# Kernel optimization log

Measured on AMD Instinct MI355X. Metric: run time of the kernel, lower is better.

Reference implementation:

```python
import jax, jax.numpy as jnp
import numpy as np

MAGNITUDE = 9
PROB = 0.5
WARP_STRENGTH = MAGNITUDE * 0.3 / 9.0  # = 0.3


def _notaknot_matrix(S):
    # System for second derivatives M of a cubic spline on uniform grid h=1
    # (scipy CubicSpline default bc_type='not-a-knot').
    A = np.zeros((S, S), dtype=np.float32)
    i = np.arange(1, S - 1)
    A[i, i - 1] = 1.0
    A[i, i] = 4.0
    A[i, i + 1] = 1.0
    # not-a-knot: third derivative continuous at x1 and x_{S-2}
    A[0, 0], A[0, 1], A[0, 2] = 1.0, -2.0, 1.0
    A[-1, -3], A[-1, -2], A[-1, -1] = 1.0, -2.0, 1.0
    return A


def setup_inputs() -> dict:
    key = jax.random.key(0)
    k1, k2, k3 = jax.random.split(key, 3)
    B, C, S = 128, 64, 4096
    x = jax.random.normal(k1, (B, C, S), dtype=jnp.float32)
    # per-sample scale ~ U(1 - warp_strength, 1 + warp_strength)
    scale = (1.0 - WARP_STRENGTH) + 2.0 * WARP_STRENGTH * jax.random.uniform(k2, (B,), dtype=jnp.float32)
    # per-sample apply decision: rand < prob
    apply_mask = jax.random.uniform(k3, (B,)) < PROB
    return {"x": x, "scale": scale, "apply_mask": apply_mask}


def reference(x, scale, apply_mask):
    B, C, S = x.shape
    A = jnp.asarray(_notaknot_matrix(S))  # (S, S), fixed uniform-grid system

    # --- fit not-a-knot cubic splines for all B*C signals at once ---
    y = x.reshape(B * C, S)
    rhs = jnp.zeros_like(y).at[:, 1:-1].set(
        6.0 * (y[:, :-2] - 2.0 * y[:, 1:-1] + y[:, 2:])
    )  # not-a-knot rows have rhs 0
    M = jnp.linalg.solve(A, rhs.T).T.reshape(B, C, S)  # second derivatives

    # --- warped evaluation points (shared across channels of a sample) ---
    grid = jnp.arange(S, dtype=x.dtype)
    w = jnp.clip(grid[None, :] * scale[:, None], 0.0, S - 1)  # (B, S)
    idx = jnp.clip(jnp.floor(w).astype(jnp.int32), 0, S - 2)  # interval index
    t = (w - idx.astype(x.dtype))[:, None, :]                 # (B, 1, S)

    idx3 = jnp.broadcast_to(idx[:, None, :], (B, C, S))
    y0 = jnp.take_along_axis(x, idx3, axis=2)
    y1 = jnp.take_along_axis(x, idx3 + 1, axis=2)
    M0 = jnp.take_along_axis(M, idx3, axis=2)
    M1 = jnp.take_along_axis(M, idx3 + 1, axis=2)

    # s(t) = y0 + b t + c t^2 + d t^3 on each unit interval (h = 1)
    b = (y1 - y0) - (2.0 * M0 + M1) / 6.0
    c = M0 / 2.0
    d = (M1 - M0) / 6.0
    warped = y0 + t * (b + t * (c + t * d))

    return jnp.where(apply_mask[:, None, None], warped, x)
```

## Files before the change

### kernel.cpp

```cpp
#include <hip/hip_runtime.h>
#include <math.h>


#define SLEN 4096
#define WRAD 8
#define BLK  256

typedef float f32x4 __attribute__((ext_vector_type(4)));

__global__ __launch_bounds__(BLK, 5) void time_warp_kernel(
    const float* __restrict__ x,
    const float* __restrict__ scale,
    const int*   __restrict__ apply_mask,
    float* __restrict__ out,
    int C)
{
    __shared__ float sy[SLEN];
    __shared__ float sm[SLEN];

    const int bid = blockIdx.x;
    const int b   = bid / C;
    const int t   = threadIdx.x;
    const float* __restrict__ xin = x   + (size_t)bid * SLEN;
    float*       __restrict__ o   = out + (size_t)bid * SLEN;

    if (apply_mask[b] == 0) {
        const f32x4* __restrict__ xi4 = (const f32x4*)xin;
        f32x4*       __restrict__ o4  = (f32x4*)o;
        #pragma unroll
        for (int k = 0; k < 4; ++k) {
            f32x4 v = xi4[t + BLK * k];
            __builtin_nontemporal_store(v, &o4[t + BLK * k]);
        }
        return;
    }

    {
        const float4* __restrict__ xi4 = (const float4*)xin;
        #pragma unroll
        for (int k = 0; k < 4; ++k)
            *(float4*)&sy[4 * (t + BLK * k)] = xi4[t + BLK * k];
    }
    __syncthreads();

    const float r = 0.26794919243112270f;
    float G[WRAD + 1];
    G[0] = 0.28867513459481287f;
    #pragma unroll
    for (int k = 1; k <= WRAD; ++k) G[k] = -G[k - 1] * r;
    float Hh[WRAD + 2];
    Hh[0] = 12.0f * (G[1] - G[0]);
    #pragma unroll
    for (int k = 1; k < WRAD; ++k) Hh[k] = 6.0f * (G[k - 1] - 2.0f * G[k] + G[k + 1]);
    Hh[WRAD]     = 6.0f * (G[WRAD - 1] - 2.0f * G[WRAD]);
    Hh[WRAD + 1] = 6.0f * G[WRAD];
    const float log2r = -1.8999686269529532f;

    #pragma unroll
    for (int s = 0; s < 4; ++s) {
        const int j0 = 4 * t + 1024 * s;
        if (j0 >= 36 && j0 <= SLEN - 44) {
            float wv[28];
            #pragma unroll
            for (int m = 0; m < 7; ++m)
                *(float4*)&wv[4 * m] = *(const float4*)&sy[j0 - 12 + 4 * m];
            float mv[4];
            #pragma unroll
            for (int e = 0; e < 4; ++e) {
                float acc = Hh[0] * wv[12 + e];
                #pragma unroll
                for (int k = 1; k <= WRAD + 1; ++k)
                    acc += Hh[k] * (wv[12 + e - k] + wv[12 + e + k]);
                mv[e] = acc;
            }
            *(float4*)&sm[j0] = make_float4(mv[0], mv[1], mv[2], mv[3]);
        } else {
            const float M1  = sy[0]        - 2.0f * sy[1]        + sy[2];
            const float MS2 = sy[SLEN - 3] - 2.0f * sy[SLEN - 2] + sy[SLEN - 1];

            float v1 = 0.0f, vS2 = 0.0f;
            #pragma unroll
            for (int k = 1; k <= WRAD; ++k) {
                const int ja = 1 + k;
                float fa = 6.0f * (sy[ja - 1] - 2.0f * sy[ja] + sy[ja + 1]);
                if (ja == 2) fa -= M1;
                v1 += G[k] * fa;
                const int jb = SLEN - 2 - k;
                float fb = 6.0f * (sy[jb - 1] - 2.0f * sy[jb] + sy[jb + 1]);
                if (jb == SLEN - 3) fb -= MS2;
                vS2 += G[k] * fb;
            }

            float wv[28];
            #pragma unroll
            for (int m = 0; m < 7; ++m) {
                const int q = j0 - 12 + 4 * m;
                float4 v = make_float4(0.0f, 0.0f, 0.0f, 0.0f);
                if (q >= 0 && q <= SLEN - 4) v = *(const float4*)&sy[q];
                *(float4*)&wv[4 * m] = v;
            }
            float fw[20];
            #pragma unroll
            for (int p = 0; p < 20; ++p) {
                const int jj = j0 + p - 8;
                float fv = 6.0f * (wv[p + 3] - 2.0f * wv[p + 4] + wv[p + 5]);
                if (jj < 2 || jj > SLEN - 3) fv = 0.0f;
                if (jj == 2)        fv -= M1;
                if (jj == SLEN - 3) fv -= MS2;
                fw[p] = fv;
            }
            float mv[4];
            #pragma unroll
            for (int e = 0; e < 4; ++e) {
                float acc = G[0] * fw[8 + e];
                #pragma unroll
                for (int k = 1; k <= WRAD; ++k)
                    acc += G[k] * (fw[8 + e - k] + fw[8 + e + k]);
                const int i = j0 + e;
                if (i >= 2 && i <= 34) {
                    float cc = v1 * exp2f((float)(i - 1) * log2r);
                    acc += (i & 1) ? -cc : cc;
                }
                if (i >= SLEN - 36 && i <= SLEN - 3) {
                    float cc = vS2 * exp2f((float)(SLEN - 2 - i) * log2r);
                    acc += (i & 1) ? cc : -cc;
                }
                mv[e] = acc;
            }
            if (j0 == 0)        { mv[1] = M1;  mv[0] = 2.0f * M1  - mv[2]; }
            if (j0 == SLEN - 4) { mv[2] = MS2; mv[3] = 2.0f * MS2 - mv[1]; }
            *(float4*)&sm[j0] = make_float4(mv[0], mv[1], mv[2], mv[3]);
        }
    }
    __syncthreads();

    const float sc = scale[b];
    #pragma unroll
    for (int q = 0; q < 16; ++q) {
        const int j = t + BLK * q;
        float w = fminf((float)j * sc, (float)(SLEN - 1));
        int idx = (int)w;
        if (idx > SLEN - 2) idx = SLEN - 2;
        const float tt  = w - (float)idx;
        const float y0  = sy[idx];
        const float y1  = sy[idx + 1];
        const float m0  = sm[idx];
        const float m1v = sm[idx + 1];
        const float bb = (y1 - y0) - (2.0f * m0 + m1v) * (1.0f / 6.0f);
        const float cc = 0.5f * m0;
        const float dd = (m1v - m0) * (1.0f / 6.0f);
        const float res = y0 + tt * (bb + tt * (cc + tt * dd));
        __builtin_nontemporal_store(res, &o[j]);
    }
}

extern "C" void kernel_launch(void* const* d_in, const int* in_sizes, int n_in,
                              void* d_out, int out_size, void* d_ws, size_t ws_size,
                              hipStream_t stream) {
    const float* x     = (const float*)d_in[0];
    const float* scale = (const float*)d_in[1];
    const int*   mask  = (const int*)d_in[2];
    float*       out   = (float*)d_out;

    const int B     = in_sizes[1];
    const int total = in_sizes[0];
    const int C     = total / (B * SLEN);
    const int nblk  = B * C;

    time_warp_kernel<<<nblk, BLK, 0, stream>>>(x, scale, mask, out, C);
}
```

Measured before the change: 237.9 us.

## Use persistent blocks with register prefetch of the next signal

The per-signal grid becomes a persistent grid of 1280 blocks that loop over signals with a stride. Each block loads the next signal into registers while it computes the spline for the current one, so global load latency overlaps with compute. Custom barriers that only wait on LDS replace __syncthreads. Masked signals are now copied from shared memory rather than directly from global memory, and holding the prefetch registers may raise register pressure and limit occupancy.

```diff
diff --git a/kernel.cpp b/kernel.cpp
--- a/kernel.cpp
+++ b/kernel.cpp
@@ -5,43 +5,28 @@
 #define SLEN 4096
 #define WRAD 8
 #define BLK  256
+#define GRID 1280
 
 typedef float f32x4 __attribute__((ext_vector_type(4)));
+
+__device__ __forceinline__ void lbar() {
+    __builtin_amdgcn_sched_barrier(0);
+    asm volatile("s_waitcnt lgkmcnt(0)" ::: "memory");
+    __builtin_amdgcn_s_barrier();
+    __builtin_amdgcn_sched_barrier(0);
+}
 
 __global__ __launch_bounds__(BLK, 5) void time_warp_kernel(
     const float* __restrict__ x,
     const float* __restrict__ scale,
     const int*   __restrict__ apply_mask,
     float* __restrict__ out,
-    int C)
+    int C, int nsig)
 {
     __shared__ float sy[SLEN];
     __shared__ float sm[SLEN];
 
-    const int bid = blockIdx.x;
-    const int b   = bid / C;
-    const int t   = threadIdx.x;
-    const float* __restrict__ xin = x   + (size_t)bid * SLEN;
-    float*       __restrict__ o   = out + (size_t)bid * SLEN;
-
-    if (apply_mask[b] == 0) {
-        const f32x4* __restrict__ xi4 = (const f32x4*)xin;
-        f32x4*       __restrict__ o4  = (f32x4*)o;
-        #pragma unroll
-        for (int k = 0; k < 4; ++k) {
-            f32x4 v = xi4[t + BLK * k];
-            __builtin_nontemporal_store(v, &o4[t + BLK * k]);
-        }
-        return;
-    }
-
-    {
-        const float4* __restrict__ xi4 = (const float4*)xin;
-        #pragma unroll
-        for (int k = 0; k < 4; ++k)
-            *(float4*)&sy[4 * (t + BLK * k)] = xi4[t + BLK * k];
-    }
-    __syncthreads();
+    const int t = threadIdx.x;
 
     const float r = 0.26794919243112270f;
     float G[WRAD + 1];
@@ -56,101 +41,142 @@
     Hh[WRAD + 1] = 6.0f * G[WRAD];
     const float log2r = -1.8999686269529532f;
 
-    #pragma unroll
-    for (int s = 0; s < 4; ++s) {
-        const int j0 = 4 * t + 1024 * s;
-        if (j0 >= 36 && j0 <= SLEN - 44) {
-            float wv[28];
+    int bid = blockIdx.x;
+    f32x4 pf0, pf1, pf2, pf3;
+    if (bid < nsig) {
+        const f32x4* __restrict__ xi4 = (const f32x4*)(x + (size_t)bid * SLEN);
+        pf0 = xi4[t];
+        pf1 = xi4[t + BLK];
+        pf2 = xi4[t + 2 * BLK];
+        pf3 = xi4[t + 3 * BLK];
+    }
+
+    for (; bid < nsig; bid += GRID) {
+        const int   b   = bid / C;
+        const int   msk = apply_mask[b];
+        const float sc  = scale[b];
+        float* __restrict__ o = out + (size_t)bid * SLEN;
+
+        lbar();
+        *(f32x4*)&sy[4 * t]        = pf0;
+        *(f32x4*)&sy[4 * t + 1024] = pf1;
+        *(f32x4*)&sy[4 * t + 2048] = pf2;
+        *(f32x4*)&sy[4 * t + 3072] = pf3;
+        lbar();
+
+        const int nxt = bid + GRID;
+        if (nxt < nsig) {
+            const f32x4* __restrict__ xi4 = (const f32x4*)(x + (size_t)nxt * SLEN);
+            pf0 = xi4[t];
+            pf1 = xi4[t + BLK];
+            pf2 = xi4[t + 2 * BLK];
+            pf3 = xi4[t + 3 * BLK];
+        }
+
+        if (msk == 0) {
             #pragma unroll
-            for (int m = 0; m < 7; ++m)
-                *(float4*)&wv[4 * m] = *(const float4*)&sy[j0 - 12 + 4 * m];
-            float mv[4];
-            #pragma unroll
-            for (int e = 0; e < 4; ++e) {
-                float acc = Hh[0] * wv[12 + e];
+            for (int k = 0; k < 4; ++k) {
+                f32x4 v = *(const f32x4*)&sy[4 * (t + BLK * k)];
+                __builtin_nontemporal_store(v, &((f32x4*)o)[t + BLK * k]);
+            }
+            continue;
+        }
+
+        #pragma unroll
+        for (int s = 0; s < 4; ++s) {
+            const int j0 = 4 * t + 1024 * s;
+            if (j0 >= 36 && j0 <= SLEN - 44) {
+                float wv[28];
                 #pragma unroll
-                for (int k = 1; k <= WRAD + 1; ++k)
-                    acc += Hh[k] * (wv[12 + e - k] + wv[12 + e + k]);
-                mv[e] = acc;
+                for (int m = 0; m < 7; ++m)
+                    *(float4*)&wv[4 * m] = *(const float4*)&sy[j0 - 12 + 4 * m];
+                float mv[4];
+                #pragma unroll
+                for (int e = 0; e < 4; ++e) {
+                    float acc = Hh[0] * wv[12 + e];
+                    #pragma unroll
+                    for (int k = 1; k <= WRAD + 1; ++k)
+                        acc += Hh[k] * (wv[12 + e - k] + wv[12 + e + k]);
+                    mv[e] = acc;
+                }
+                *(float4*)&sm[j0] = make_float4(mv[0], mv[1], mv[2], mv[3]);
+            } else {
+                const float M1  = sy[0]        - 2.0f * sy[1]        + sy[2];
+                const float MS2 = sy[SLEN - 3] - 2.0f * sy[SLEN - 2] + sy[SLEN - 1];
+
+                float v1 = 0.0f, vS2 = 0.0f;
+                #pragma unroll
+                for (int k = 1; k <= WRAD; ++k) {
+                    const int ja = 1 + k;
+                    float fa = 6.0f * (sy[ja - 1] - 2.0f * sy[ja] + sy[ja + 1]);
+                    if (ja == 2) fa -= M1;
+                    v1 += G[k] * fa;
+                    const int jb = SLEN - 2 - k;
+                    float fb = 6.0f * (sy[jb - 1] - 2.0f * sy[jb] + sy[jb + 1]);
+                    if (jb == SLEN - 3) fb -= MS2;
+                    vS2 += G[k] * fb;
+                }
+
+                float wv[28];
+                #pragma unroll
+                for (int m = 0; m < 7; ++m) {
+                    const int q = j0 - 12 + 4 * m;
+                    float4 v = make_float4(0.0f, 0.0f, 0.0f, 0.0f);
+                    if (q >= 0 && q <= SLEN - 4) v = *(const float4*)&sy[q];
+                    *(float4*)&wv[4 * m] = v;
+                }
+                float fw[20];
+                #pragma unroll
+                for (int p = 0; p < 20; ++p) {
+                    const int jj = j0 + p - 8;
+                    float fv = 6.0f * (wv[p + 3] - 2.0f * wv[p + 4] + wv[p + 5]);
+                    if (jj < 2 || jj > SLEN - 3) fv = 0.0f;
+                    if (jj == 2)        fv -= M1;
+                    if (jj == SLEN - 3) fv -= MS2;
+                    fw[p] = fv;
+                }
+                float mv[4];
+                #pragma unroll
+                for (int e = 0; e < 4; ++e) {
+                    float acc = G[0] * fw[8 + e];
+                    #pragma unroll
+                    for (int k = 1; k <= WRAD; ++k)
+                        acc += G[k] * (fw[8 + e - k] + fw[8 + e + k]);
+                    const int i = j0 + e;
+                    if (i >= 2 && i <= 34) {
+                        float cc = v1 * exp2f((float)(i - 1) * log2r);
+                        acc += (i & 1) ? -cc : cc;
+                    }
+                    if (i >= SLEN - 36 && i <= SLEN - 3) {
+                        float cc = vS2 * exp2f((float)(SLEN - 2 - i) * log2r);
+                        acc += (i & 1) ? cc : -cc;
+                    }
+                    mv[e] = acc;
+                }
+                if (j0 == 0)        { mv[1] = M1;  mv[0] = 2.0f * M1  - mv[2]; }
+                if (j0 == SLEN - 4) { mv[2] = MS2; mv[3] = 2.0f * MS2 - mv[1]; }
+                *(float4*)&sm[j0] = make_float4(mv[0], mv[1], mv[2], mv[3]);
             }
-            *(float4*)&sm[j0] = make_float4(mv[0], mv[1], mv[2], mv[3]);
-        } else {
-            const float M1  = sy[0]        - 2.0f * sy[1]        + sy[2];
-            const float MS2 = sy[SLEN - 3] - 2.0f * sy[SLEN - 2] + sy[SLEN - 1];
+        }
+        lbar();
 
-            float v1 = 0.0f, vS2 = 0.0f;
-            #pragma unroll
-            for (int k = 1; k <= WRAD; ++k) {
-                const int ja = 1 + k;
-                float fa = 6.0f * (sy[ja - 1] - 2.0f * sy[ja] + sy[ja + 1]);
-                if (ja == 2) fa -= M1;
-                v1 += G[k] * fa;
-                const int jb = SLEN - 2 - k;
-                float fb = 6.0f * (sy[jb - 1] - 2.0f * sy[jb] + sy[jb + 1]);
-                if (jb == SLEN - 3) fb -= MS2;
-                vS2 += G[k] * fb;
-            }
-
-            float wv[28];
-            #pragma unroll
-            for (int m = 0; m < 7; ++m) {
-                const int q = j0 - 12 + 4 * m;
-                float4 v = make_float4(0.0f, 0.0f, 0.0f, 0.0f);
-                if (q >= 0 && q <= SLEN - 4) v = *(const float4*)&sy[q];
-                *(float4*)&wv[4 * m] = v;
-            }
-            float fw[20];
-            #pragma unroll
-            for (int p = 0; p < 20; ++p) {
-                const int jj = j0 + p - 8;
-                float fv = 6.0f * (wv[p + 3] - 2.0f * wv[p + 4] + wv[p + 5]);
-                if (jj < 2 || jj > SLEN - 3) fv = 0.0f;
-                if (jj == 2)        fv -= M1;
-                if (jj == SLEN - 3) fv -= MS2;
-                fw[p] = fv;
-            }
-            float mv[4];
-            #pragma unroll
-            for (int e = 0; e < 4; ++e) {
-                float acc = G[0] * fw[8 + e];
-                #pragma unroll
-                for (int k = 1; k <= WRAD; ++k)
-                    acc += G[k] * (fw[8 + e - k] + fw[8 + e + k]);
-                const int i = j0 + e;
-                if (i >= 2 && i <= 34) {
-                    float cc = v1 * exp2f((float)(i - 1) * log2r);
-                    acc += (i & 1) ? -cc : cc;
-                }
-                if (i >= SLEN - 36 && i <= SLEN - 3) {
-                    float cc = vS2 * exp2f((float)(SLEN - 2 - i) * log2r);
-                    acc += (i & 1) ? cc : -cc;
-                }
-                mv[e] = acc;
-            }
-            if (j0 == 0)        { mv[1] = M1;  mv[0] = 2.0f * M1  - mv[2]; }
-            if (j0 == SLEN - 4) { mv[2] = MS2; mv[3] = 2.0f * MS2 - mv[1]; }
-            *(float4*)&sm[j0] = make_float4(mv[0], mv[1], mv[2], mv[3]);
+        #pragma unroll
+        for (int q = 0; q < 16; ++q) {
+            const int j = t + BLK * q;
+            float w = fminf((float)j * sc, (float)(SLEN - 1));
+            int idx = (int)w;
+            if (idx > SLEN - 2) idx = SLEN - 2;
+            const float tt  = w - (float)idx;
+            const float y0  = sy[idx];
+            const float y1  = sy[idx + 1];
+            const float m0  = sm[idx];
+            const float m1v = sm[idx + 1];
+            const float bb = (y1 - y0) - (2.0f * m0 + m1v) * (1.0f / 6.0f);
+            const float cc = 0.5f * m0;
+            const float dd = (m1v - m0) * (1.0f / 6.0f);
+            const float res = y0 + tt * (bb + tt * (cc + tt * dd));
+            __builtin_nontemporal_store(res, &o[j]);
         }
-    }
-    __syncthreads();
-
-    const float sc = scale[b];
-    #pragma unroll
-    for (int q = 0; q < 16; ++q) {
-        const int j = t + BLK * q;
-        float w = fminf((float)j * sc, (float)(SLEN - 1));
-        int idx = (int)w;
-        if (idx > SLEN - 2) idx = SLEN - 2;
-        const float tt  = w - (float)idx;
-        const float y0  = sy[idx];
-        const float y1  = sy[idx + 1];
-        const float m0  = sm[idx];
-        const float m1v = sm[idx + 1];
-        const float bb = (y1 - y0) - (2.0f * m0 + m1v) * (1.0f / 6.0f);
-        const float cc = 0.5f * m0;
-        const float dd = (m1v - m0) * (1.0f / 6.0f);
-        const float res = y0 + tt * (bb + tt * (cc + tt * dd));
-        __builtin_nontemporal_store(res, &o[j]);
     }
 }
 
@@ -165,7 +191,8 @@
     const int B     = in_sizes[1];
     const int total = in_sizes[0];
     const int C     = total / (B * SLEN);
-    const int nblk  = B * C;
+    const int nsig  = B * C;
 
-    time_warp_kernel<<<nblk, BLK, 0, stream>>>(x, scale, mask, out, C);
+    const int grid = (nsig < GRID) ? nsig : GRID;
+    time_warp_kernel<<<grid, BLK, 0, stream>>>(x, scale, mask, out, C, nsig);
 }
```

New measurement: 259.6 us. 1.09x slower.

## Fuse spline second-derivative computation into warped evaluation, drop shared M buffer

Applied to the files above, without the earlier changes.

Instead of computing the second derivatives for every sample into a shared array and then gathering from it, each thread now computes only the M values its four warped outputs need, using a window of y around the warped index, and writes the outputs as float4. This removes the sm shared array, one barrier and the separate gather pass, and cuts LDS use, which may raise occupancy. In exchange the stencil is evaluated on unaligned scalar LDS reads. Edge cases go to a noinline helper that recomputes the boundary terms per output, which is costly but rarely taken.

```diff
diff --git a/kernel.cpp b/kernel.cpp
--- a/kernel.cpp
+++ b/kernel.cpp
@@ -7,6 +7,97 @@
 #define BLK  256
 
 typedef float f32x4 __attribute__((ext_vector_type(4)));
+
+__device__ __attribute__((noinline))
+f32x4 edge_eval(const float* __restrict__ sy, int j0, float sc)
+{
+    const float log2r = -1.8999686269529532f;
+    const float r = 0.26794919243112270f;
+    float G[WRAD + 1];
+    G[0] = 0.28867513459481287f;
+    #pragma unroll
+    for (int k = 1; k <= WRAD; ++k) G[k] = -G[k - 1] * r;
+
+    const float M1  = sy[0]        - 2.0f * sy[1]        + sy[2];
+    const float MS2 = sy[SLEN - 3] - 2.0f * sy[SLEN - 2] + sy[SLEN - 1];
+
+    float v1 = 0.0f, vS2 = 0.0f;
+    #pragma unroll
+    for (int k = 1; k <= WRAD; ++k) {
+        const int ja = 1 + k;
+        float fa = 6.0f * (sy[ja - 1] - 2.0f * sy[ja] + sy[ja + 1]);
+        if (ja == 2) fa -= M1;
+        v1 += G[k] * fa;
+        const int jb = SLEN - 2 - k;
+        float fb = 6.0f * (sy[jb - 1] - 2.0f * sy[jb] + sy[jb + 1]);
+        if (jb == SLEN - 3) fb -= MS2;
+        vS2 += G[k] * fb;
+    }
+
+    auto Mconv = [&](int i) -> float {
+        float acc = 0.0f;
+        #pragma unroll
+        for (int k = -WRAD; k <= WRAD; ++k) {
+            const int j = i + k;
+            float fj = 0.0f;
+            if (j >= 2 && j <= SLEN - 3) {
+                fj = 6.0f * (sy[j - 1] - 2.0f * sy[j] + sy[j + 1]);
+                if (j == 2)        fj -= M1;
+                if (j == SLEN - 3) fj -= MS2;
+            }
+            acc += G[k < 0 ? -k : k] * fj;
+        }
+        if (i <= 34) {
+            float cc = v1 * exp2f((float)(i - 1) * log2r);
+            acc += (i & 1) ? -cc : cc;
+        }
+        if (i >= SLEN - 36) {
+            float cc = vS2 * exp2f((float)(SLEN - 2 - i) * log2r);
+            acc += (i & 1) ? cc : -cc;
+        }
+        return acc;
+    };
+    auto Mfull = [&](int i) -> float {
+        if (i == 1)        return M1;
+        if (i == SLEN - 2) return MS2;
+        if (i == 0)        return 2.0f * M1  - Mconv(2);
+        if (i == SLEN - 1) return 2.0f * MS2 - Mconv(SLEN - 3);
+        return Mconv(i);
+    };
+
+    f32x4 rv;
+    float w0 = fminf((float)j0 * sc, (float)(SLEN - 1));
+    int  id0 = (int)w0; if (id0 > SLEN - 2) id0 = SLEN - 2;
+    if (id0 == SLEN - 2) {
+        const float m0 = MS2;
+        const float m1 = 2.0f * MS2 - Mconv(SLEN - 3);
+        const float y0 = sy[SLEN - 2], y1 = sy[SLEN - 1];
+        const float bb = (y1 - y0) - (2.0f * m0 + m1) * (1.0f / 6.0f);
+        const float cf = 0.5f * m0;
+        const float dd = (m1 - m0) * (1.0f / 6.0f);
+        #pragma unroll
+        for (int e = 0; e < 4; ++e) {
+            float w  = fminf((float)(j0 + e) * sc, (float)(SLEN - 1));
+            float tt = w - (float)(SLEN - 2);
+            rv[e] = y0 + tt * (bb + tt * (cf + tt * dd));
+        }
+        return rv;
+    }
+    #pragma unroll
+    for (int e = 0; e < 4; ++e) {
+        float w  = fminf((float)(j0 + e) * sc, (float)(SLEN - 1));
+        int  id  = (int)w; if (id > SLEN - 2) id = SLEN - 2;
+        const float tt = w - (float)id;
+        const float m0 = Mfull(id);
+        const float m1 = Mfull(id + 1);
+        const float y0 = sy[id], y1 = sy[id + 1];
+        const float bb = (y1 - y0) - (2.0f * m0 + m1) * (1.0f / 6.0f);
+        const float cf = 0.5f * m0;
+        const float dd = (m1 - m0) * (1.0f / 6.0f);
+        rv[e] = y0 + tt * (bb + tt * (cf + tt * dd));
+    }
+    return rv;
+}
 
 __global__ __launch_bounds__(BLK, 5) void time_warp_kernel(
     const float* __restrict__ x,
@@ -16,7 +107,6 @@
     int C)
 {
     __shared__ float sy[SLEN];
-    __shared__ float sm[SLEN];
 
     const int bid = blockIdx.x;
     const int b   = bid / C;
@@ -43,6 +133,8 @@
     }
     __syncthreads();
 
+    const float sc = scale[b];
+
     const float r = 0.26794919243112270f;
     float G[WRAD + 1];
     G[0] = 0.28867513459481287f;
@@ -54,103 +146,51 @@
     for (int k = 1; k < WRAD; ++k) Hh[k] = 6.0f * (G[k - 1] - 2.0f * G[k] + G[k + 1]);
     Hh[WRAD]     = 6.0f * (G[WRAD - 1] - 2.0f * G[WRAD]);
     Hh[WRAD + 1] = 6.0f * G[WRAD];
-    const float log2r = -1.8999686269529532f;
 
     #pragma unroll
     for (int s = 0; s < 4; ++s) {
         const int j0 = 4 * t + 1024 * s;
-        if (j0 >= 36 && j0 <= SLEN - 44) {
-            float wv[28];
+        const int idx0 = (int)fminf((float)j0 * sc, (float)(SLEN - 1));
+        f32x4 res;
+
+        if (idx0 >= 35 && idx0 <= SLEN - 42) {
+            const float* __restrict__ wp = &sy[idx0 - 9];
+            float wv[24];
             #pragma unroll
-            for (int m = 0; m < 7; ++m)
-                *(float4*)&wv[4 * m] = *(const float4*)&sy[j0 - 12 + 4 * m];
-            float mv[4];
+            for (int m = 0; m < 24; ++m) wv[m] = wp[m];
+
+            float Ms[6];
+            #pragma unroll
+            for (int ii = 0; ii < 6; ++ii) {
+                float acc = Hh[0] * wv[9 + ii];
+                #pragma unroll
+                for (int k = 1; k <= WRAD + 1; ++k)
+                    acc += Hh[k] * (wv[9 + ii - k] + wv[9 + ii + k]);
+                Ms[ii] = acc;
+            }
+
             #pragma unroll
             for (int e = 0; e < 4; ++e) {
-                float acc = Hh[0] * wv[12 + e];
-                #pragma unroll
-                for (int k = 1; k <= WRAD + 1; ++k)
-                    acc += Hh[k] * (wv[12 + e - k] + wv[12 + e + k]);
-                mv[e] = acc;
+                const float w  = (float)(j0 + e) * sc;
+                const int   id = (int)w;
+                const float tt = w - (float)id;
+                const int   d  = id - idx0;
+                float m0 = Ms[0], m1 = Ms[1];
+                if (d >= 1) { m0 = Ms[1]; m1 = Ms[2]; }
+                if (d >= 2) { m0 = Ms[2]; m1 = Ms[3]; }
+                if (d >= 3) { m0 = Ms[3]; m1 = Ms[4]; }
+                if (d >= 4) { m0 = Ms[4]; m1 = Ms[5]; }
+                const float y0 = sy[id], y1 = sy[id + 1];
+                const float bb = (y1 - y0) - (2.0f * m0 + m1) * (1.0f / 6.0f);
+                const float cf = 0.5f * m0;
+                const float dd = (m1 - m0) * (1.0f / 6.0f);
+                res[e] = y0 + tt * (bb + tt * (cf + tt * dd));
             }
-            *(float4*)&sm[j0] = make_float4(mv[0], mv[1], mv[2], mv[3]);
         } else {
-            const float M1  = sy[0]        - 2.0f * sy[1]        + sy[2];
-            const float MS2 = sy[SLEN - 3] - 2.0f * sy[SLEN - 2] + sy[SLEN - 1];
-
-            float v1 = 0.0f, vS2 = 0.0f;
-            #pragma unroll
-            for (int k = 1; k <= WRAD; ++k) {
-                const int ja = 1 + k;
-                float fa = 6.0f * (sy[ja - 1] - 2.0f * sy[ja] + sy[ja + 1]);
-                if (ja == 2) fa -= M1;
-                v1 += G[k] * fa;
-                const int jb = SLEN - 2 - k;
-                float fb = 6.0f * (sy[jb - 1] - 2.0f * sy[jb] + sy[jb + 1]);
-                if (jb == SLEN - 3) fb -= MS2;
-                vS2 += G[k] * fb;
-            }
-
-            float wv[28];
-            #pragma unroll
-            for (int m = 0; m < 7; ++m) {
-                const int q = j0 - 12 + 4 * m;
-                float4 v = make_float4(0.0f, 0.0f, 0.0f, 0.0f);
-                if (q >= 0 && q <= SLEN - 4) v = *(const float4*)&sy[q];
-                *(float4*)&wv[4 * m] = v;
-            }
-            float fw[20];
-            #pragma unroll
-            for (int p = 0; p < 20; ++p) {
-                const int jj = j0 + p - 8;
-                float fv = 6.0f * (wv[p + 3] - 2.0f * wv[p + 4] + wv[p + 5]);
-                if (jj < 2 || jj > SLEN - 3) fv = 0.0f;
-                if (jj == 2)        fv -= M1;
-                if (jj == SLEN - 3) fv -= MS2;
-                fw[p] = fv;
-            }
-            float mv[4];
-            #pragma unroll
-            for (int e = 0; e < 4; ++e) {
-                float acc = G[0] * fw[8 + e];
-                #pragma unroll
-                for (int k = 1; k <= WRAD; ++k)
-                    acc += G[k] * (fw[8 + e - k] + fw[8 + e + k]);
-                const int i = j0 + e;
-                if (i >= 2 && i <= 34) {
-                    float cc = v1 * exp2f((float)(i - 1) * log2r);
-                    acc += (i & 1) ? -cc : cc;
-                }
-                if (i >= SLEN - 36 && i <= SLEN - 3) {
-                    float cc = vS2 * exp2f((float)(SLEN - 2 - i) * log2r);
-                    acc += (i & 1) ? cc : -cc;
-                }
-                mv[e] = acc;
-            }
-            if (j0 == 0)        { mv[1] = M1;  mv[0] = 2.0f * M1  - mv[2]; }
-            if (j0 == SLEN - 4) { mv[2] = MS2; mv[3] = 2.0f * MS2 - mv[1]; }
-            *(float4*)&sm[j0] = make_float4(mv[0], mv[1], mv[2], mv[3]);
-        }
-    }
-    __syncthreads();
-
-    const float sc = scale[b];
-    #pragma unroll
-    for (int q = 0; q < 16; ++q) {
-        const int j = t + BLK * q;
-        float w = fminf((float)j * sc, (float)(SLEN - 1));
-        int idx = (int)w;
-        if (idx > SLEN - 2) idx = SLEN - 2;
-        const float tt  = w - (float)idx;
-        const float y0  = sy[idx];
-        const float y1  = sy[idx + 1];
-        const float m0  = sm[idx];
-        const float m1v = sm[idx + 1];
-        const float bb = (y1 - y0) - (2.0f * m0 + m1v) * (1.0f / 6.0f);
-        const float cc = 0.5f * m0;
-        const float dd = (m1v - m0) * (1.0f / 6.0f);
-        const float res = y0 + tt * (bb + tt * (cc + tt * dd));
-        __builtin_nontemporal_store(res, &o[j]);
+            res = edge_eval(sy, j0, sc);
+        }
+
+        __builtin_nontemporal_store(res, (f32x4*)&o[j0]);
     }
 }
 
```

New measurement: 259.2 us. +9.0%, slower.

## Interleave y and M in shared memory and shorten interior spline filter

Applied to the files above, without the earlier changes.

Stores each sample and its second derivative as an interleaved float2 in shared memory, so evaluation fetches two 8-byte LDS reads instead of four 4-byte ones. It also cuts the interior IIR-approximation filter radius from 8 to 6 taps, reducing ALU and LDS load work. Shared memory per block grows from 32KB to 48KB, so the launch-bounds occupancy hint drops from 5 to 3 blocks. The shorter filter truncates the geometric kernel earlier, which trades some accuracy for less work.

```diff
diff --git a/kernel.cpp b/kernel.cpp
--- a/kernel.cpp
+++ b/kernel.cpp
@@ -4,19 +4,20 @@
 
 #define SLEN 4096
 #define WRAD 8
+#define WC   6
 #define BLK  256
 
 typedef float f32x4 __attribute__((ext_vector_type(4)));
 
-__global__ __launch_bounds__(BLK, 5) void time_warp_kernel(
+__global__ __launch_bounds__(BLK, 3) void time_warp_kernel(
     const float* __restrict__ x,
     const float* __restrict__ scale,
     const int*   __restrict__ apply_mask,
     float* __restrict__ out,
     int C)
 {
-    __shared__ float sy[SLEN];
-    __shared__ float sm[SLEN];
+    __shared__ float  sy[SLEN];
+    __shared__ float2 sym2[SLEN];
 
     const int bid = blockIdx.x;
     const int b   = bid / C;
@@ -48,32 +49,33 @@
     G[0] = 0.28867513459481287f;
     #pragma unroll
     for (int k = 1; k <= WRAD; ++k) G[k] = -G[k - 1] * r;
-    float Hh[WRAD + 2];
+    float Hh[WC + 2];
     Hh[0] = 12.0f * (G[1] - G[0]);
     #pragma unroll
-    for (int k = 1; k < WRAD; ++k) Hh[k] = 6.0f * (G[k - 1] - 2.0f * G[k] + G[k + 1]);
-    Hh[WRAD]     = 6.0f * (G[WRAD - 1] - 2.0f * G[WRAD]);
-    Hh[WRAD + 1] = 6.0f * G[WRAD];
+    for (int k = 1; k < WC; ++k) Hh[k] = 6.0f * (G[k - 1] - 2.0f * G[k] + G[k + 1]);
+    Hh[WC]     = 6.0f * (G[WC - 1] - 2.0f * G[WC]);
+    Hh[WC + 1] = 6.0f * G[WC];
     const float log2r = -1.8999686269529532f;
 
     #pragma unroll
     for (int s = 0; s < 4; ++s) {
         const int j0 = 4 * t + 1024 * s;
         if (j0 >= 36 && j0 <= SLEN - 44) {
-            float wv[28];
+            float wv[20];
             #pragma unroll
-            for (int m = 0; m < 7; ++m)
-                *(float4*)&wv[4 * m] = *(const float4*)&sy[j0 - 12 + 4 * m];
+            for (int m = 0; m < 5; ++m)
+                *(float4*)&wv[4 * m] = *(const float4*)&sy[j0 - 8 + 4 * m];
             float mv[4];
             #pragma unroll
             for (int e = 0; e < 4; ++e) {
-                float acc = Hh[0] * wv[12 + e];
+                float acc = Hh[0] * wv[8 + e];
                 #pragma unroll
-                for (int k = 1; k <= WRAD + 1; ++k)
-                    acc += Hh[k] * (wv[12 + e - k] + wv[12 + e + k]);
+                for (int k = 1; k <= WC + 1; ++k)
+                    acc += Hh[k] * (wv[8 + e - k] + wv[8 + e + k]);
                 mv[e] = acc;
             }
-            *(float4*)&sm[j0] = make_float4(mv[0], mv[1], mv[2], mv[3]);
+            *(float4*)&sym2[j0]     = make_float4(wv[8],  mv[0], wv[9],  mv[1]);
+            *(float4*)&sym2[j0 + 2] = make_float4(wv[10], mv[2], wv[11], mv[3]);
         } else {
             const float M1  = sy[0]        - 2.0f * sy[1]        + sy[2];
             const float MS2 = sy[SLEN - 3] - 2.0f * sy[SLEN - 2] + sy[SLEN - 1];
@@ -129,7 +131,8 @@
             }
             if (j0 == 0)        { mv[1] = M1;  mv[0] = 2.0f * M1  - mv[2]; }
             if (j0 == SLEN - 4) { mv[2] = MS2; mv[3] = 2.0f * MS2 - mv[1]; }
-            *(float4*)&sm[j0] = make_float4(mv[0], mv[1], mv[2], mv[3]);
+            *(float4*)&sym2[j0]     = make_float4(wv[12], mv[0], wv[13], mv[1]);
+            *(float4*)&sym2[j0 + 2] = make_float4(wv[14], mv[2], wv[15], mv[3]);
         }
     }
     __syncthreads();
@@ -141,14 +144,14 @@
         float w = fminf((float)j * sc, (float)(SLEN - 1));
         int idx = (int)w;
         if (idx > SLEN - 2) idx = SLEN - 2;
-        const float tt  = w - (float)idx;
-        const float y0  = sy[idx];
-        const float y1  = sy[idx + 1];
-        const float m0  = sm[idx];
-        const float m1v = sm[idx + 1];
-        const float bb = (y1 - y0) - (2.0f * m0 + m1v) * (1.0f / 6.0f);
+        const float tt = w - (float)idx;
+        const float2 p0 = sym2[idx];
+        const float2 p1 = sym2[idx + 1];
+        const float y0 = p0.x, m0 = p0.y;
+        const float y1 = p1.x, m1 = p1.y;
+        const float bb = (y1 - y0) - (2.0f * m0 + m1) * (1.0f / 6.0f);
         const float cc = 0.5f * m0;
-        const float dd = (m1v - m0) * (1.0f / 6.0f);
+        const float dd = (m1 - m0) * (1.0f / 6.0f);
         const float res = y0 + tt * (bb + tt * (cc + tt * dd));
         __builtin_nontemporal_store(res, &o[j]);
     }
```

Result: no change. 234.2 us (-1.5%).
